# Optimization experiments

Hardware: AMD Instinct MI355X
Metric: run time of the kernel (lower is better)

The kernel has to match this reference:

```python
import jax, jax.numpy as jnp
import numpy as np

B, D, DEPTH, H, E, N, NC = 128, 192, 12, 3, 4, 65, 100
WIN_HALF = 3  # window_size=7 -> |i-j| <= 3


def _ln(x, g, b, eps=1e-5):
    m = x.mean(-1, keepdims=True)
    v = ((x - m) ** 2).mean(-1, keepdims=True)
    return (x - m) / jnp.sqrt(v + eps) * g + b


def _forward(x, conv_w, conv_b, pe_g, pe_b, cls_token, pos_embed,
             n1_g, n1_b, qkv_w, temp, proj_w, proj_b, n2_g, n2_b,
             gate_w, gate_b, e_w1, e_b1, e_w2, e_b2, attn_scale, mlp_scale,
             norm_g, norm_b, hc_w, hc_b, head_w, head_b):
    Bx = x.shape[0]
    # patch embed: conv with kernel==stride==4 is a blocked matmul
    p = x.reshape(Bx, 3, 8, 4, 8, 4).transpose(0, 2, 4, 1, 3, 5).reshape(Bx, 64, 48)
    t = p @ conv_w.reshape(D, 48).T + conv_b
    t = _ln(t, pe_g, pe_b)
    t = jnp.concatenate([jnp.broadcast_to(cls_token, (Bx, 1, D)), t], axis=1) + pos_embed
    Nn = t.shape[1]
    hd = D // H
    scale = hd ** -0.5
    idx = jnp.arange(Nn)
    # local-window attention mask (log of {0,1} -> {-inf,0})
    mask = jnp.where(jnp.abs(idx[:, None] - idx[None, :]) <= WIN_HALF, 0.0, -jnp.inf)
    for l in range(DEPTH):
        # --- attention ---
        y = _ln(t, n1_g[l], n1_b[l])
        qkv = (y @ qkv_w[l].T).reshape(Bx, Nn, 3, H, hd).transpose(2, 0, 3, 1, 4)
        q, k, v = qkv[0], qkv[1], qkv[2]
        a = (q @ k.transpose(0, 1, 3, 2)) * scale / temp[l]  # [B,H,N,N]
        a = jax.nn.softmax(a + mask, axis=-1)
        o = (a @ v).transpose(0, 2, 1, 3).reshape(Bx, Nn, D)
        o = o @ proj_w[l].T + proj_b[l]
        t = t + attn_scale[l] * o
        # --- top-2 MoE (dense-equivalent of the masked per-expert dispatch) ---
        y = _ln(t, n2_g[l], n2_b[l])
        g = jax.nn.softmax(y @ gate_w[l].T + gate_b[l], axis=-1)  # [B,N,E]
        tg, ti = jax.lax.top_k(g, 2)
        tg = tg / tg.sum(-1, keepdims=True)
        h = jax.nn.gelu(jnp.einsum('bnc,ehc->bneh', y, e_w1[l]) + e_b1[l], approximate=False)
        eo = jnp.einsum('bneh,ech->bnec', h, e_w2[l]) + e_b2[l]  # [B,N,E,C]
        sel = jnp.take_along_axis(eo, ti[..., None], axis=2)  # [B,N,2,C]
        mo = (sel * tg[..., None]).sum(axis=2)
        t = t + mlp_scale[l] * mo
    t = _ln(t, norm_g, norm_b)
    cls = t[:, 0]
    # hypercomplex linear head: out[:,k] += x[:,j] @ W[(k-j)%n].T
    xv = cls.reshape(Bx, E, D // E)
    perm = (jnp.arange(E)[:, None] - jnp.arange(E)[None, :]) % E  # [k,j] -> i
    hh = jnp.einsum('bjc,kjoc->bko', xv, hc_w[perm]).reshape(Bx, 2 * D) + hc_b
    hh = jax.nn.gelu(hh, approximate=False)
    return hh @ head_w.T + head_b


def setup_inputs() -> dict:
    ks = iter(jax.random.split(jax.random.key(0), 64))
    def rn(shape, s=0.02):
        return jax.random.normal(next(ks), shape, jnp.float32) * s
    return dict(
        x=jax.random.normal(next(ks), (B, 3, 32, 32), jnp.float32),
        conv_w=rn((D, 3, 4, 4)), conv_b=jnp.zeros((D,)),
        pe_g=jnp.ones((D,)), pe_b=jnp.zeros((D,)),
        cls_token=rn((1, 1, D)), pos_embed=rn((1, N, D)),
        n1_g=jnp.ones((DEPTH, D)), n1_b=jnp.zeros((DEPTH, D)),
        qkv_w=rn((DEPTH, 3 * D, D)), temp=jnp.ones((DEPTH, H, 1, 1)),
        proj_w=rn((DEPTH, D, D)), proj_b=jnp.zeros((DEPTH, D)),
        n2_g=jnp.ones((DEPTH, D)), n2_b=jnp.zeros((DEPTH, D)),
        gate_w=rn((DEPTH, E, D)), gate_b=jnp.zeros((DEPTH, E)),
        e_w1=rn((DEPTH, E, 2 * D, D)), e_b1=jnp.zeros((DEPTH, E, 2 * D)),
        e_w2=rn((DEPTH, E, D, 2 * D)), e_b2=jnp.zeros((DEPTH, E, D)),
        attn_scale=jnp.ones((DEPTH,)), mlp_scale=jnp.ones((DEPTH,)),
        norm_g=jnp.ones((D,)), norm_b=jnp.zeros((D,)),
        hc_w=rn((E, 2 * D // E, D // E)), hc_b=jnp.zeros((2 * D,)),
        head_w=rn((NC, 2 * D)), head_b=jnp.zeros((NC,)),
    )


def reference(x, conv_w, conv_b, pe_g, pe_b, cls_token, pos_embed,
              n1_g, n1_b, qkv_w, temp, proj_w, proj_b, n2_g, n2_b,
              gate_w, gate_b, e_w1, e_b1, e_w2, e_b2, attn_scale, mlp_scale,
              norm_g, norm_b, hc_w, hc_b, head_w, head_b):
    return _forward(x, conv_w, conv_b, pe_g, pe_b, cls_token, pos_embed,
                    n1_g, n1_b, qkv_w, temp, proj_w, proj_b, n2_g, n2_b,
                    gate_w, gate_b, e_w1, e_b1, e_w2, e_b2, attn_scale, mlp_scale,
                    norm_g, norm_b, hc_w, hc_b, head_w, head_b)
```

## Files before the change

kernel.cpp:

```cpp
#include <hip/hip_runtime.h>
#include <cmath>

#define ROWS 8320
#define DD   192

typedef __attribute__((ext_vector_type(8))) _Float16 half8;
typedef __attribute__((ext_vector_type(4))) float floatx4;

#define GLD16(gp, lp) __builtin_amdgcn_global_load_lds( \
    (const __attribute__((address_space(1))) void*)(gp), \
    (__attribute__((address_space(3))) void*)(lp), 16, 0, 0)

#define MFMA_F16 __builtin_amdgcn_mfma_f32_16x16x32_f16

__device__ __forceinline__ float gelu_f(float x) {
    return 0.5f * x * (1.0f + erff(x * 0.70710678118654752440f));
}

__device__ __forceinline__ float blk_sum_192(float v, float* sbuf) {
    int tid = threadIdx.x;
    sbuf[tid] = v;
    __syncthreads();
    for (int off = 96; off >= 3; off >>= 1) {
        if (tid < off) sbuf[tid] += sbuf[tid + off];
        __syncthreads();
    }
    float r = sbuf[0] + sbuf[1] + sbuf[2];
    __syncthreads();
    return r;
}

__global__ __launch_bounds__(256) void cvt_h_kernel(
    const float* __restrict__ s, _Float16* __restrict__ d, long n8)
{
    long i = (long)blockIdx.x * 256 + threadIdx.x;
    if (i >= n8) return;
    const float* sp = s + i * 8;
    _Float16* dp = d + i * 8;
    #pragma unroll
    for (int j = 0; j < 8; j++) dp[j] = (_Float16)sp[j];
}

__global__ __launch_bounds__(256) void permw2h_kernel(
    const float* __restrict__ s, _Float16* __restrict__ d)
{
    long i = (long)blockIdx.x * 256 + threadIdx.x;
    if (i >= (long)12 * 192 * 192) return;
    int l = (int)(i / (192 * 192));
    int rem = (int)(i % (192 * 192));
    int n = rem / 192, p = rem % 192;
    int c0 = p * 8;
    int e = c0 / 384, k0 = c0 % 384;
    const float* sp = s + (((size_t)l * 4 + e) * 192 + n) * 384 + k0;
    _Float16* dp = d + i * 8;
    #pragma unroll
    for (int j = 0; j < 8; j++) dp[j] = (_Float16)sp[j];
}

__global__ __launch_bounds__(192) void embed_kernel(
    const float* __restrict__ x, const float* __restrict__ conv_w,
    const float* __restrict__ conv_b, const float* __restrict__ pe_g,
    const float* __restrict__ pe_b, const float* __restrict__ cls_tok,
    const float* __restrict__ pos, float* __restrict__ t)
{
    __shared__ float patch[48];
    __shared__ float red[192];
    int blk = blockIdx.x;
    int b = blk / 65, n = blk % 65;
    int tid = threadIdx.x;
    if (n == 0) {
        t[(size_t)b * 65 * DD + tid] = cls_tok[tid] + pos[tid];
        return;
    }
    int p = n - 1, gy = p / 8, gx = p % 8;
    if (tid < 48) {
        int c = tid / 16, iy = (tid % 16) / 4, ix = tid % 4;
        patch[tid] = x[((size_t)b * 3 + c) * 1024 + (size_t)(gy * 4 + iy) * 32 + (gx * 4 + ix)];
    }
    __syncthreads();
    float s = conv_b[tid];
    const float* w = conv_w + (size_t)tid * 48;
    #pragma unroll
    for (int f = 0; f < 48; f++) s += patch[f] * w[f];
    float mean = blk_sum_192(s, red) * (1.0f / 192.0f);
    float d = s - mean;
    float var = blk_sum_192(d * d, red) * (1.0f / 192.0f);
    float o = d * rsqrtf(var + 1e-5f) * pe_g[tid] + pe_b[tid];
    t[((size_t)b * 65 + n) * DD + tid] = o + pos[(size_t)n * DD + tid];
}

__global__ __launch_bounds__(256) void ln_kernel(
    const float* __restrict__ in, const float* __restrict__ ctb,
    float* __restrict__ tout,
    float* __restrict__ yf, _Float16* __restrict__ yh,
    const float* __restrict__ g, const float* __restrict__ bb, long in_stride, int nrows,
    const float* __restrict__ gwm, const float* __restrict__ gb,
    int4* __restrict__ gwout)
{
    int wave = threadIdx.x >> 6, lane = threadIdx.x & 63;
    int r = blockIdx.x * 4 + wave;
    if (r >= nrows) return;
    const float* row = in + (size_t)r * in_stride;
    float v0 = row[lane], v1 = row[lane + 64], v2 = row[lane + 128];
    if (ctb) {
        long gr = (long)r * (in_stride / DD);
        const float* cb = ctb + gr * 384;
        v0 += cb[lane] + cb[192 + lane];
        v1 += cb[lane + 64] + cb[256 + lane];
        v2 += cb[lane + 128] + cb[320 + lane];
        if (tout) {
            float* tr = tout + (size_t)r * in_stride;
            tr[lane] = v0; tr[lane + 64] = v1; tr[lane + 128] = v2;
        }
    }
    float s = v0 + v1 + v2;
    #pragma unroll
    for (int off = 32; off > 0; off >>= 1) s += __shfl_xor(s, off);
    float mean = s * (1.0f / 192.0f);
    float d0 = v0 - mean, d1 = v1 - mean, d2 = v2 - mean;
    float q = d0 * d0 + d1 * d1 + d2 * d2;
    #pragma unroll
    for (int off = 32; off > 0; off >>= 1) q += __shfl_xor(q, off);
    float rstd = rsqrtf(q * (1.0f / 192.0f) + 1e-5f);
    float o0 = d0 * rstd * g[lane] + bb[lane];
    float o1 = d1 * rstd * g[lane + 64] + bb[lane + 64];
    float o2 = d2 * rstd * g[lane + 128] + bb[lane + 128];
    if (yf) {
        float* yr = yf + (size_t)r * DD;
        yr[lane] = o0; yr[lane + 64] = o1; yr[lane + 128] = o2;
    }
    if (yh) {
        _Float16* yr = yh + (size_t)r * DD;
        yr[lane] = (_Float16)o0; yr[lane + 64] = (_Float16)o1; yr[lane + 128] = (_Float16)o2;
    }
    if (gwm) {
        float pe[4];
        #pragma unroll
        for (int e = 0; e < 4; e++) {
            const float* w = gwm + (size_t)e * DD;
            pe[e] = o0 * w[lane] + o1 * w[lane + 64] + o2 * w[lane + 128];
            #pragma unroll
            for (int off = 32; off > 0; off >>= 1) pe[e] += __shfl_xor(pe[e], off);
        }
        if (lane == 0) {
            #pragma unroll
            for (int e = 0; e < 4; e++) pe[e] += gb[e];
            float mx = fmaxf(fmaxf(pe[0], pe[1]), fmaxf(pe[2], pe[3]));
            float ex[4];
            #pragma unroll
            for (int e = 0; e < 4; e++) ex[e] = expf(pe[e] - mx);
            int i0 = 0;
            #pragma unroll
            for (int e = 1; e < 4; e++) if (ex[e] > ex[i0]) i0 = e;
            int i1 = (i0 == 0) ? 1 : 0;
            #pragma unroll
            for (int e = 0; e < 4; e++) if (e != i0 && ex[e] > ex[i1]) i1 = e;
            float denom = ex[i0] + ex[i1];
            int4 o4;
            o4.x = i0; o4.y = i1;
            o4.z = __float_as_int(ex[i0] / denom);
            o4.w = __float_as_int(ex[i1] / denom);
            gwout[r] = o4;
        }
    }
}

__global__ __launch_bounds__(256) void gate_build_kernel(
    const int4* __restrict__ gwrow, int* __restrict__ cnt,
    int* __restrict__ list, float* __restrict__ wlist, int rows)
{
    int r = blockIdx.x * 256 + threadIdx.x;
    int lane = threadIdx.x & 63;
    bool active = r < rows;
    int4 gv = active ? gwrow[r] : int4{-1, -1, 0, 0};
    #pragma unroll
    for (int e = 0; e < 4; e++) {
        bool sel = active && (gv.x == e || gv.y == e);
        float w = (gv.x == e) ? __int_as_float(gv.z) : __int_as_float(gv.w);
        unsigned long long mask = __ballot(sel);
        int cw = __popcll(mask);
        if (cw) {
            int leader = __ffsll((long long)mask) - 1;
            int base = 0;
            if (lane == leader) base = atomicAdd(&cnt[e], cw);
            base = __shfl(base, leader);
            if (sel) {
                int idx = base + __popcll(mask & ((1ULL << lane) - 1ULL));
                int rank = (gv.x == e) ? 0 : 1;
                list[(size_t)e * ROWS + idx] = (r << 1) | rank;
                wlist[(size_t)e * ROWS + idx] = w;
            }
        }
    }
}

template <int MODE>
__global__ __launch_bounds__(256) void gemm_h(
    const _Float16* __restrict__ A, const _Float16* __restrict__ W,
    int Nn, _Float16* __restrict__ outH, float* __restrict__ t,
    const float* __restrict__ bias, const float* __restrict__ scale)
{
    __shared__ __align__(16) _Float16 As[64 * 192];
    __shared__ __align__(16) _Float16 Ws[64 * 192];
    const int tid = threadIdx.x;
    const int lane = tid & 63, wave = tid >> 6;
    const int m0 = blockIdx.x * 64, n0 = blockIdx.y * 64;
    const int wm = (wave & 1) * 32, wn = (wave >> 1) * 32;
    const int lr = lane & 15, quad = lane >> 4;

    #pragma unroll
    for (int i = 0; i < 6; i++) {
        int s = (wave * 6 + i) * 64 + lane;
        int rr = s / 24, c = s % 24;
        GLD16(A + (size_t)(m0 + rr) * 192 + (c ^ (rr & 7)) * 8,
              (char*)As + (size_t)(wave * 6 + i) * 1024);
        GLD16(W + (size_t)(n0 + rr) * 192 + (c ^ (rr & 7)) * 8,
              (char*)Ws + (size_t)(wave * 6 + i) * 1024);
    }
    __syncthreads();

    floatx4 zero = {0.f, 0.f, 0.f, 0.f};
    floatx4 acc[2][2];
    acc[0][0] = zero; acc[0][1] = zero; acc[1][0] = zero; acc[1][1] = zero;

    #pragma unroll
    for (int m = 0; m < 6; m++) {
        int ch = m * 4 + quad;
        half8 a[2], w[2];
        #pragma unroll
        for (int ti = 0; ti < 2; ti++) {
            int ar = wm + ti * 16 + lr;
            a[ti] = *(const half8*)(As + ((size_t)ar * 24 + (ch ^ (ar & 7))) * 8);
            int cr = wn + ti * 16 + lr;
            w[ti] = *(const half8*)(Ws + ((size_t)cr * 24 + (ch ^ (cr & 7))) * 8);
        }
        #pragma unroll
        for (int ti = 0; ti < 2; ti++)
            #pragma unroll
            for (int tj = 0; tj < 2; tj++)
                acc[ti][tj] = MFMA_F16(a[ti], w[tj], acc[ti][tj], 0, 0, 0);
    }

    float sc = (MODE == 2) ? scale[0] : 0.f;
    #pragma unroll
    for (int ti = 0; ti < 2; ti++)
        #pragma unroll
        for (int tj = 0; tj < 2; tj++)
            #pragma unroll
            for (int r = 0; r < 4; r++) {
                int grow = m0 + wm + ti * 16 + quad * 4 + r;
                int gcol = n0 + wn + tj * 16 + lr;
                float v = acc[ti][tj][r];
                if (MODE == 0) {
                    float vp = __shfl_xor(v, 1);
                    if ((lane & 1) == 0) {
                        union { _Float16 h[2]; unsigned u; } pk;
                        pk.h[0] = (_Float16)v;
                        pk.h[1] = (_Float16)vp;
                        *(unsigned*)(outH + (size_t)grow * Nn + (gcol & ~1)) = pk.u;
                    }
                } else {
                    t[(size_t)grow * DD + gcol] += sc * (v + bias[gcol]);
                }
            }
}

__global__ __launch_bounds__(256) void moe_kernel(
    const _Float16* __restrict__ yh, const _Float16* __restrict__ w1,
    const _Float16* __restrict__ w2, const float* __restrict__ b1,
    const float* __restrict__ b2, const float* __restrict__ scale,
    const int* __restrict__ cnt, const int* __restrict__ list,
    const float* __restrict__ wlist, float* __restrict__ t)
{
    __shared__ __align__(16) _Float16 W1s[64 * 192];
    __shared__ __align__(16) _Float16 W2s[192 * 64];
    __shared__ __align__(16) _Float16 Hs[32 * 64];
    const int e  = blockIdx.y;
    const int cnte = cnt[e];
    const int r0 = blockIdx.x * 32;
    if (r0 >= cnte) return;
    const int tid = threadIdx.x;
    const int lane = tid & 63, wave = tid >> 6;
    const int lr = lane & 15, quad = lane >> 4;
    const int wr = (wave & 1) * 16;
    const int wc1 = (wave >> 1) * 16;
    const int wc2 = (wave >> 1) * 96;

    #pragma unroll
    for (int i = 0; i < 6; i++) {
        int s = (wave * 6 + i) * 64 + lane;
        int rr = s / 24, c = s % 24;
        GLD16(w1 + ((size_t)e * 384 + rr) * 192 + (c ^ (rr & 7)) * 8,
              (char*)W1s + (size_t)(wave * 6 + i) * 1024);
    }

    int sl = r0 + wr + lr;
    int rv = -1; float wv = 0.f;
    if (sl < cnte) {
        rv = list[(size_t)e * ROWS + sl];
        wv = wlist[(size_t)e * ROWS + sl];
    }
    int arow = (rv >= 0) ? (rv >> 1) : 0;

    half8 a[6];
    {
        const _Float16* ap = yh + (size_t)arow * 192 + quad * 8;
        #pragma unroll
        for (int m = 0; m < 6; m++) a[m] = *(const half8*)(ap + m * 32);
    }

    int rvr[4]; float bwr[4];
    #pragma unroll
    for (int r = 0; r < 4; r++) {
        rvr[r] = __shfl(rv, quad * 4 + r);
        bwr[r] = __shfl(wv, quad * 4 + r);
    }

    __syncthreads();

    floatx4 zero = {0.f, 0.f, 0.f, 0.f};
    floatx4 acc2[6];
    #pragma unroll
    for (int j = 0; j < 6; j++) acc2[j] = zero;

    for (int nc = 0; nc < 6; nc++) {
        int ncg = e * 6 + nc;
        #pragma unroll
        for (int i = 0; i < 6; i++) {
            int s = (wave * 6 + i) * 64 + lane;
            int n = s >> 3, c = s & 7;
            GLD16(w2 + (size_t)n * 1536 + (ncg * 8 + (c ^ (n & 7))) * 8,
                  (char*)W2s + (size_t)(wave * 6 + i) * 1024);
        }
        floatx4 acc1[2];
        acc1[0] = zero; acc1[1] = zero;
        #pragma unroll
        for (int m = 0; m < 6; m++) {
            int ch = m * 4 + quad;
            #pragma unroll
            for (int tc = 0; tc < 2; tc++) {
                int cr = wc1 + tc * 32 + lr;
                half8 w = *(const half8*)(W1s + ((size_t)cr * 24 + (ch ^ (cr & 7))) * 8);
                acc1[tc] = MFMA_F16(a[m], w, acc1[tc], 0, 0, 0);
            }
        }
        #pragma unroll
        for (int tc = 0; tc < 2; tc++)
            #pragma unroll
            for (int r = 0; r < 4; r++) {
                int hrow = wr + quad * 4 + r;
                int hcol = wc1 + tc * 32 + lr;
                float v = gelu_f(acc1[tc][r] + b1[64 * ncg + hcol]) * bwr[r];
                float vp = __shfl_xor(v, 1);
                if ((lane & 1) == 0) {
                    union { _Float16 h[2]; unsigned u; } pk;
                    pk.h[0] = (_Float16)v;
                    pk.h[1] = (_Float16)vp;
                    int cl = (hcol >> 3) ^ (hrow & 7);
                    *(unsigned*)(Hs + ((size_t)hrow * 8 + cl) * 8 + (hcol & 7)) = pk.u;
                }
            }
        __syncthreads();
        if (nc < 5) {
            #pragma unroll
            for (int i = 0; i < 6; i++) {
                int s = (wave * 6 + i) * 64 + lane;
                int rr = s / 24, c = s % 24;
                GLD16(w1 + ((size_t)e * 384 + (nc + 1) * 64 + rr) * 192 + (c ^ (rr & 7)) * 8,
                      (char*)W1s + (size_t)(wave * 6 + i) * 1024);
            }
        }
        #pragma unroll
        for (int kk = 0; kk < 2; kk++) {
            int ar = wr + lr;
            int ch = kk * 4 + quad;
            half8 ha = *(const half8*)(Hs + ((size_t)ar * 8 + (ch ^ (ar & 7))) * 8);
            #pragma unroll
            for (int tj = 0; tj < 6; tj++) {
                int cr = wc2 + tj * 16 + lr;
                half8 w = *(const half8*)(W2s + ((size_t)cr * 8 + (ch ^ (cr & 7))) * 8);
                acc2[tj] = MFMA_F16(ha, w, acc2[tj], 0, 0, 0);
            }
        }
        __syncthreads();
    }

    float sc = scale[0];
    #pragma unroll
    for (int tj = 0; tj < 6; tj++) {
        int gcol = wc2 + tj * 16 + lr;
        float b2v = b2[e * 192 + gcol];
        #pragma unroll
        for (int r = 0; r < 4; r++) {
            if (rvr[r] >= 0) {
                float v = sc * (acc2[tj][r] + bwr[r] * b2v);
                atomicAdd(&t[(size_t)(rvr[r] >> 1) * DD + gcol], v);
            }
        }
    }
}

__global__ __launch_bounds__(256) void attn_kernel(
    const _Float16* __restrict__ qkv, const float* __restrict__ temp,
    _Float16* __restrict__ o)
{
    __shared__ float q[65][65], k[65][65], v[65][65];
    __shared__ float p[65][8];
    int bh = blockIdx.x;
    int b = bh / 3, h = bh % 3;
    int tid = threadIdx.x;
    float coef = 0.125f / temp[h];
    const _Float16* base = qkv + (size_t)b * 65 * 576 + h * 64;
    for (int idx = tid; idx < 65 * 64; idx += 256) {
        int i = idx >> 6, d = idx & 63;
        q[i][d] = (float)base[(size_t)i * 576 + d];
        k[i][d] = (float)base[(size_t)i * 576 + 192 + d];
        v[i][d] = (float)base[(size_t)i * 576 + 384 + d];
    }
    __syncthreads();
    if (tid < 65) {
        int i = tid;
        float sc[7];
        float mx = -1e30f;
        #pragma unroll
        for (int jo = 0; jo < 7; jo++) {
            int j = i - 3 + jo;
            if (j >= 0 && j < 65) {
                float s = 0.f;
                #pragma unroll
                for (int d = 0; d < 64; d++) s += q[i][d] * k[j][d];
                sc[jo] = s * coef;
                mx = fmaxf(mx, sc[jo]);
            } else sc[jo] = -1e30f;
        }
        float sum = 0.f;
        #pragma unroll
        for (int jo = 0; jo < 7; jo++) {
            float e = expf(sc[jo] - mx);
            p[i][jo] = e;
            sum += e;
        }
        float inv = 1.0f / sum;
        #pragma unroll
        for (int jo = 0; jo < 7; jo++) p[i][jo] *= inv;
    }
    __syncthreads();
    for (int idx = tid; idx < 65 * 64; idx += 256) {
        int i = idx >> 6, d = idx & 63;
        float s = 0.f;
        #pragma unroll
        for (int jo = 0; jo < 7; jo++) {
            int j = i - 3 + jo;
            if (j >= 0 && j < 65) s += p[i][jo] * v[j][d];
        }
        o[((size_t)b * 65 + i) * 192 + h * 64 + d] = (_Float16)s;
    }
}

__global__ __launch_bounds__(128) void head_kernel(
    const float* __restrict__ cls, const float* __restrict__ hc_w,
    const float* __restrict__ hc_b, const float* __restrict__ head_w,
    const float* __restrict__ head_b, float* __restrict__ out)
{
    __shared__ float c[192];
    __shared__ float hh[384];
    int b = blockIdx.x, tid = threadIdx.x;
    for (int i = tid; i < 192; i += 128) c[i] = cls[(size_t)b * 192 + i];
    __syncthreads();
    for (int i = tid; i < 384; i += 128) {
        int kx = i / 96, o = i % 96;
        float s = hc_b[i];
        #pragma unroll
        for (int j = 0; j < 4; j++) {
            int pp = (kx - j + 4) & 3;
            const float* w = hc_w + ((size_t)pp * 96 + o) * 48;
            const float* xv = c + j * 48;
            #pragma unroll
            for (int cc = 0; cc < 48; cc++) s += xv[cc] * w[cc];
        }
        hh[i] = gelu_f(s);
    }
    __syncthreads();
    for (int i = tid; i < 100; i += 128) {
        float s = head_b[i];
        const float* w = head_w + (size_t)i * 384;
        for (int kk = 0; kk < 384; kk++) s += hh[kk] * w[kk];
        out[(size_t)b * 100 + i] = s;
    }
}

extern "C" void kernel_launch(void* const* d_in, const int* in_sizes, int n_in,
                              void* d_out, int out_size, void* d_ws, size_t ws_size,
                              hipStream_t stream)
{
    const float* x        = (const float*)d_in[0];
    const float* conv_w   = (const float*)d_in[1];
    const float* conv_b   = (const float*)d_in[2];
    const float* pe_g     = (const float*)d_in[3];
    const float* pe_b     = (const float*)d_in[4];
    const float* cls_tok  = (const float*)d_in[5];
    const float* pos      = (const float*)d_in[6];
    const float* n1_g     = (const float*)d_in[7];
    const float* n1_b     = (const float*)d_in[8];
    const float* qkv_w    = (const float*)d_in[9];
    const float* temp     = (const float*)d_in[10];
    const float* proj_w   = (const float*)d_in[11];
    const float* proj_b   = (const float*)d_in[12];
    const float* n2_g     = (const float*)d_in[13];
    const float* n2_b     = (const float*)d_in[14];
    const float* gate_w   = (const float*)d_in[15];
    const float* gate_b   = (const float*)d_in[16];
    const float* e_w1     = (const float*)d_in[17];
    const float* e_b1     = (const float*)d_in[18];
    const float* e_w2     = (const float*)d_in[19];
    const float* e_b2     = (const float*)d_in[20];
    const float* attn_sc  = (const float*)d_in[21];
    const float* mlp_sc   = (const float*)d_in[22];
    const float* norm_g   = (const float*)d_in[23];
    const float* norm_b   = (const float*)d_in[24];
    const float* hc_w     = (const float*)d_in[25];
    const float* hc_b     = (const float*)d_in[26];
    const float* head_w   = (const float*)d_in[27];
    const float* head_b   = (const float*)d_in[28];

    char* base = (char*)d_ws;
    float*  t     = (float*)base;   base += (size_t)ROWS * DD * 4;
    int4*   gwrow = (int4*)base;    base += (size_t)ROWS * 16;
    int*    cnts  = (int*)base;     base += (size_t)12 * 4 * sizeof(int) + 64;
    int*    elist = (int*)base;     base += (size_t)4 * ROWS * 4;
    float*  ewls  = (float*)base;   base += (size_t)4 * ROWS * 4;
    float*  ycls  = (float*)base;   base += (size_t)128 * DD * 4;
    _Float16* yhb = (_Float16*)base; base += (size_t)ROWS * DD * 2;
    _Float16* qkvh = (_Float16*)base; base += (size_t)ROWS * 576 * 2;
    _Float16* osph = (_Float16*)base; base += (size_t)ROWS * DD * 2;
    _Float16* qkvw_h = (_Float16*)base; base += (size_t)12 * 576 * 192 * 2;
    _Float16* projw_h = (_Float16*)base; base += (size_t)12 * 192 * 192 * 2;
    _Float16* ew1_h = (_Float16*)base; base += (size_t)12 * 1536 * 192 * 2;
    _Float16* ew2_h = (_Float16*)base; base += (size_t)12 * 192 * 1536 * 2;

    hipMemsetAsync(cnts, 0, 12 * 4 * sizeof(int), stream);

    {
        long n8 = (long)12 * 576 * 192 / 8;
        cvt_h_kernel<<<(int)((n8 + 255) / 256), 256, 0, stream>>>(qkv_w, qkvw_h, n8);
        n8 = (long)12 * 192 * 192 / 8;
        cvt_h_kernel<<<(int)((n8 + 255) / 256), 256, 0, stream>>>(proj_w, projw_h, n8);
        n8 = (long)12 * 1536 * 192 / 8;
        cvt_h_kernel<<<(int)((n8 + 255) / 256), 256, 0, stream>>>(e_w1, ew1_h, n8);
        long n = (long)12 * 192 * 192;
        permw2h_kernel<<<(int)((n + 255) / 256), 256, 0, stream>>>(e_w2, ew2_h);
    }

    embed_kernel<<<128 * 65, 192, 0, stream>>>(x, conv_w, conv_b, pe_g, pe_b, cls_tok, pos, t);

    for (int l = 0; l < 12; l++) {
        ln_kernel<<<ROWS / 4, 256, 0, stream>>>(
            t, nullptr, nullptr,
            nullptr, yhb, n1_g + l * DD, n1_b + l * DD, DD, ROWS,
            nullptr, nullptr, nullptr);
        gemm_h<0><<<dim3(130, 9), 256, 0, stream>>>(
            yhb, qkvw_h + (size_t)l * 576 * 192, 576, qkvh, nullptr, nullptr, nullptr);
        attn_kernel<<<128 * 3, 256, 0, stream>>>(qkvh, temp + l * 3, osph);
        gemm_h<2><<<dim3(130, 3), 256, 0, stream>>>(
            osph, projw_h + (size_t)l * 192 * 192, 192, nullptr, t,
            proj_b + l * DD, attn_sc + l);
        ln_kernel<<<ROWS / 4, 256, 0, stream>>>(
            t, nullptr, nullptr, nullptr, yhb, n2_g + l * DD, n2_b + l * DD, DD, ROWS,
            gate_w + (size_t)l * 4 * DD, gate_b + l * 4, gwrow);
        gate_build_kernel<<<(ROWS + 255) / 256, 256, 0, stream>>>(
            gwrow, cnts + l * 4, elist, ewls, ROWS);
        moe_kernel<<<dim3(260, 4), 256, 0, stream>>>(
            yhb, ew1_h + (size_t)l * 1536 * 192, ew2_h + (size_t)l * 192 * 1536,
            e_b1 + (size_t)l * 1536, e_b2 + (size_t)l * 4 * 192, mlp_sc + l,
            cnts + l * 4, elist, ewls, t);
    }

    ln_kernel<<<32, 256, 0, stream>>>(
        t, nullptr, nullptr, ycls, nullptr, norm_g, norm_b, (long)65 * DD, 128,
        nullptr, nullptr, nullptr);
    head_kernel<<<128, 128, 0, stream>>>(ycls, hc_w, hc_b, head_w, head_b, (float*)d_out);
}
```

Before: 1.152 ms.

## Merge weight-conversion kernels, load GEMM A tiles to registers, drop unused LN path

The four weight fp32-to-fp16 conversion launches become one combined kernel that dispatches on a flat index. In gemm_h the A operand is no longer staged through LDS; each wave loads its own A fragments straight from global memory into registers, which halves the shared-memory footprint and may raise occupancy. The unused residual-add branch in ln_kernel is removed and a loop-invariant in gate_build is hoisted. The cost is uncoalesced, non-async A loads and higher register pressure in the GEMM.

```diff
diff --git a/kernel.cpp b/kernel.cpp
--- a/kernel.cpp
+++ b/kernel.cpp
@@ -30,31 +30,36 @@
     return r;
 }
 
-__global__ __launch_bounds__(256) void cvt_h_kernel(
-    const float* __restrict__ s, _Float16* __restrict__ d, long n8)
+__device__ __forceinline__ void cvt8(const float* __restrict__ sp, _Float16* __restrict__ dp) {
+    #pragma unroll
+    for (int j = 0; j < 8; j++) dp[j] = (_Float16)sp[j];
+}
+
+__global__ __launch_bounds__(256) void cvt_all_kernel(
+    const float* __restrict__ qkv_w, const float* __restrict__ proj_w,
+    const float* __restrict__ e_w1, const float* __restrict__ e_w2,
+    _Float16* __restrict__ qkvw_h, _Float16* __restrict__ projw_h,
+    _Float16* __restrict__ ew1_h, _Float16* __restrict__ ew2_h)
 {
     long i = (long)blockIdx.x * 256 + threadIdx.x;
-    if (i >= n8) return;
-    const float* sp = s + i * 8;
-    _Float16* dp = d + i * 8;
-    #pragma unroll
-    for (int j = 0; j < 8; j++) dp[j] = (_Float16)sp[j];
-}
-
-__global__ __launch_bounds__(256) void permw2h_kernel(
-    const float* __restrict__ s, _Float16* __restrict__ d)
-{
-    long i = (long)blockIdx.x * 256 + threadIdx.x;
-    if (i >= (long)12 * 192 * 192) return;
-    int l = (int)(i / (192 * 192));
-    int rem = (int)(i % (192 * 192));
-    int n = rem / 192, p = rem % 192;
-    int c0 = p * 8;
-    int e = c0 / 384, k0 = c0 % 384;
-    const float* sp = s + (((size_t)l * 4 + e) * 192 + n) * 384 + k0;
-    _Float16* dp = d + i * 8;
-    #pragma unroll
-    for (int j = 0; j < 8; j++) dp[j] = (_Float16)sp[j];
+    const long n_qkv  = (long)12 * 576 * 192 / 8;
+    const long n_proj = (long)12 * 192 * 192 / 8;
+    const long n_w1   = (long)12 * 1536 * 192 / 8;
+    const long n_w2   = (long)12 * 192 * 192;
+    if (i < n_qkv) { cvt8(qkv_w + i * 8, qkvw_h + i * 8); return; }
+    i -= n_qkv;
+    if (i < n_proj) { cvt8(proj_w + i * 8, projw_h + i * 8); return; }
+    i -= n_proj;
+    if (i < n_w1) { cvt8(e_w1 + i * 8, ew1_h + i * 8); return; }
+    i -= n_w1;
+    if (i < n_w2) {
+        int l = (int)(i / (192 * 192));
+        int rem = (int)(i % (192 * 192));
+        int n = rem / 192, p = rem % 192;
+        int c0 = p * 8;
+        int e = c0 / 384, k0 = c0 % 384;
+        cvt8(e_w2 + (((size_t)l * 4 + e) * 192 + n) * 384 + k0, ew2_h + i * 8);
+    }
 }
 
 __global__ __launch_bounds__(192) void embed_kernel(
@@ -90,8 +95,7 @@
 }
 
 __global__ __launch_bounds__(256) void ln_kernel(
-    const float* __restrict__ in, const float* __restrict__ ctb,
-    float* __restrict__ tout,
+    const float* __restrict__ in,
     float* __restrict__ yf, _Float16* __restrict__ yh,
     const float* __restrict__ g, const float* __restrict__ bb, long in_stride, int nrows,
     const float* __restrict__ gwm, const float* __restrict__ gb,
@@ -102,17 +106,6 @@
     if (r >= nrows) return;
     const float* row = in + (size_t)r * in_stride;
     float v0 = row[lane], v1 = row[lane + 64], v2 = row[lane + 128];
-    if (ctb) {
-        long gr = (long)r * (in_stride / DD);
-        const float* cb = ctb + gr * 384;
-        v0 += cb[lane] + cb[192 + lane];
-        v1 += cb[lane + 64] + cb[256 + lane];
-        v2 += cb[lane + 128] + cb[320 + lane];
-        if (tout) {
-            float* tr = tout + (size_t)r * in_stride;
-            tr[lane] = v0; tr[lane + 64] = v1; tr[lane + 128] = v2;
-        }
-    }
     float s = v0 + v1 + v2;
     #pragma unroll
     for (int off = 32; off > 0; off >>= 1) s += __shfl_xor(s, off);
@@ -176,6 +169,7 @@
     #pragma unroll
     for (int e = 0; e < 4; e++) {
         bool sel = active && (gv.x == e || gv.y == e);
+        int rank = (gv.x == e) ? 0 : 1;
         float w = (gv.x == e) ? __int_as_float(gv.z) : __int_as_float(gv.w);
         unsigned long long mask = __ballot(sel);
         int cw = __popcll(mask);
@@ -186,7 +180,6 @@
             base = __shfl(base, leader);
             if (sel) {
                 int idx = base + __popcll(mask & ((1ULL << lane) - 1ULL));
-                int rank = (gv.x == e) ? 0 : 1;
                 list[(size_t)e * ROWS + idx] = (r << 1) | rank;
                 wlist[(size_t)e * ROWS + idx] = w;
             }
@@ -200,7 +193,6 @@
     int Nn, _Float16* __restrict__ outH, float* __restrict__ t,
     const float* __restrict__ bias, const float* __restrict__ scale)
 {
-    __shared__ __align__(16) _Float16 As[64 * 192];
     __shared__ __align__(16) _Float16 Ws[64 * 192];
     const int tid = threadIdx.x;
     const int lane = tid & 63, wave = tid >> 6;
@@ -212,10 +204,15 @@
     for (int i = 0; i < 6; i++) {
         int s = (wave * 6 + i) * 64 + lane;
         int rr = s / 24, c = s % 24;
-        GLD16(A + (size_t)(m0 + rr) * 192 + (c ^ (rr & 7)) * 8,
-              (char*)As + (size_t)(wave * 6 + i) * 1024);
         GLD16(W + (size_t)(n0 + rr) * 192 + (c ^ (rr & 7)) * 8,
               (char*)Ws + (size_t)(wave * 6 + i) * 1024);
+    }
+    half8 a[2][6];
+    #pragma unroll
+    for (int ti = 0; ti < 2; ti++) {
+        const _Float16* ap = A + (size_t)(m0 + wm + ti * 16 + lr) * 192 + quad * 8;
+        #pragma unroll
+        for (int m = 0; m < 6; m++) a[ti][m] = *(const half8*)(ap + m * 32);
     }
     __syncthreads();
 
@@ -226,19 +223,17 @@
     #pragma unroll
     for (int m = 0; m < 6; m++) {
         int ch = m * 4 + quad;
-        half8 a[2], w[2];
-        #pragma unroll
-        for (int ti = 0; ti < 2; ti++) {
-            int ar = wm + ti * 16 + lr;
-            a[ti] = *(const half8*)(As + ((size_t)ar * 24 + (ch ^ (ar & 7))) * 8);
-            int cr = wn + ti * 16 + lr;
-            w[ti] = *(const half8*)(Ws + ((size_t)cr * 24 + (ch ^ (cr & 7))) * 8);
+        half8 w[2];
+        #pragma unroll
+        for (int tj = 0; tj < 2; tj++) {
+            int cr = wn + tj * 16 + lr;
+            w[tj] = *(const half8*)(Ws + ((size_t)cr * 24 + (ch ^ (cr & 7))) * 8);
         }
         #pragma unroll
         for (int ti = 0; ti < 2; ti++)
             #pragma unroll
             for (int tj = 0; tj < 2; tj++)
-                acc[ti][tj] = MFMA_F16(a[ti], w[tj], acc[ti][tj], 0, 0, 0);
+                acc[ti][tj] = MFMA_F16(a[ti][m], w[tj], acc[ti][tj], 0, 0, 0);
     }
 
     float sc = (MODE == 2) ? scale[0] : 0.f;
@@ -541,22 +536,17 @@
     hipMemsetAsync(cnts, 0, 12 * 4 * sizeof(int), stream);
 
     {
-        long n8 = (long)12 * 576 * 192 / 8;
-        cvt_h_kernel<<<(int)((n8 + 255) / 256), 256, 0, stream>>>(qkv_w, qkvw_h, n8);
-        n8 = (long)12 * 192 * 192 / 8;
-        cvt_h_kernel<<<(int)((n8 + 255) / 256), 256, 0, stream>>>(proj_w, projw_h, n8);
-        n8 = (long)12 * 1536 * 192 / 8;
-        cvt_h_kernel<<<(int)((n8 + 255) / 256), 256, 0, stream>>>(e_w1, ew1_h, n8);
-        long n = (long)12 * 192 * 192;
-        permw2h_kernel<<<(int)((n + 255) / 256), 256, 0, stream>>>(e_w2, ew2_h);
+        long total = (long)12 * 576 * 192 / 8 + (long)12 * 192 * 192 / 8
+                   + (long)12 * 1536 * 192 / 8 + (long)12 * 192 * 192;
+        cvt_all_kernel<<<(int)((total + 255) / 256), 256, 0, stream>>>(
+            qkv_w, proj_w, e_w1, e_w2, qkvw_h, projw_h, ew1_h, ew2_h);
     }
 
     embed_kernel<<<128 * 65, 192, 0, stream>>>(x, conv_w, conv_b, pe_g, pe_b, cls_tok, pos, t);
 
     for (int l = 0; l < 12; l++) {
         ln_kernel<<<ROWS / 4, 256, 0, stream>>>(
-            t, nullptr, nullptr,
-            nullptr, yhb, n1_g + l * DD, n1_b + l * DD, DD, ROWS,
+            t, nullptr, yhb, n1_g + l * DD, n1_b + l * DD, DD, ROWS,
             nullptr, nullptr, nullptr);
         gemm_h<0><<<dim3(130, 9), 256, 0, stream>>>(
             yhb, qkvw_h + (size_t)l * 576 * 192, 576, qkvh, nullptr, nullptr, nullptr);
@@ -565,7 +555,7 @@
             osph, projw_h + (size_t)l * 192 * 192, 192, nullptr, t,
             proj_b + l * DD, attn_sc + l);
         ln_kernel<<<ROWS / 4, 256, 0, stream>>>(
-            t, nullptr, nullptr, nullptr, yhb, n2_g + l * DD, n2_b + l * DD, DD, ROWS,
+            t, nullptr, yhb, n2_g + l * DD, n2_b + l * DD, DD, ROWS,
             gate_w + (size_t)l * 4 * DD, gate_b + l * 4, gwrow);
         gate_build_kernel<<<(ROWS + 255) / 256, 256, 0, stream>>>(
             gwrow, cnts + l * 4, elist, ewls, ROWS);
@@ -576,7 +566,7 @@
     }
 
     ln_kernel<<<32, 256, 0, stream>>>(
-        t, nullptr, nullptr, ycls, nullptr, norm_g, norm_b, (long)65 * DD, 128,
+        t, ycls, nullptr, norm_g, norm_b, (long)65 * DD, 128,
         nullptr, nullptr, nullptr);
     head_kernel<<<128, 128, 0, stream>>>(ycls, hc_w, hc_b, head_w, head_b, (float*)d_out);
 }
```

Measured after the change: 1.195 ms. 1.04x slower.
